# Performance work log

Hardware: AMD Instinct MI355X
Metric: run time of the kernel (lower is better)

## Reference

```python
import jax, jax.numpy as jnp
import numpy as np

N1 = 1_000_000
N2 = 1_000_000
C = 64
M = 1_500_000


def setup_inputs() -> dict:
    key = jax.random.key(0)
    k1, k2, k3, k4, k5, k6 = jax.random.split(key, 6)
    feat1 = jax.random.normal(k1, (N1, C), dtype=jnp.float32)
    feat2 = jax.random.normal(k2, (N2, C), dtype=jnp.float32)
    # union_map[0] gathers each input row exactly once -> permutation
    map1_in = jax.random.permutation(k3, N1).astype(jnp.int32)
    map2_in = jax.random.permutation(k4, N2).astype(jnp.int32)
    # union_map[1]: output row each input point lands in
    map1_out = jax.random.randint(k5, (N1,), 0, M, dtype=jnp.int32)
    map2_out = jax.random.randint(k6, (N2,), 0, M, dtype=jnp.int32)
    return {
        "feat1": feat1, "feat2": feat2,
        "map1_in": map1_in, "map1_out": map1_out,
        "map2_in": map2_in, "map2_out": map2_out,
        "out_size": M,
    }


def reference(feat1, feat2, map1_in, map1_out, map2_in, map2_out, out_size):
    # out_feat[union_map[1]] += in_feat[union_map[0]] for each input tensor
    out = jnp.zeros((out_size, feat1.shape[1]), dtype=feat1.dtype)
    out = out.at[map1_out].add(feat1[map1_in])
    out = out.at[map2_out].add(feat2[map2_in])
    return out
```

## Files before the change

kernel.cpp:

```cpp
#include <hip/hip_runtime.h>


#define ROW_C 64
#define TBIT (1 << 30)
#define CONT 0x80000000u
#define NIL  0xFFFFFFFFu
#define SCAN_T 256
#define SCAN_PER 16
#define SCAN_CHUNK (SCAN_T * SCAN_PER)

typedef float f32x4 __attribute__((ext_vector_type(4)));
typedef int   i32x4 __attribute__((ext_vector_type(4)));
typedef unsigned long long u64;

__device__ __forceinline__ f32x4 feat_load(const float* __restrict__ feat1,
                                           const float* __restrict__ feat2,
                                           int v, int sub) {
    const float* f = (v & TBIT) ? feat2 : feat1;
    int ir = v & (TBIT - 1);
    return *reinterpret_cast<const f32x4*>(f + (size_t)ir * ROW_C + sub);
}

__global__ __launch_bounds__(256) void k_fill_list(
        const int* __restrict__ m1i, const int* __restrict__ m1o,
        const int* __restrict__ m2i, const int* __restrict__ m2o,
        int n1, int n2,
        unsigned* __restrict__ head, u64* __restrict__ entries) {
    int i = blockIdx.x * blockDim.x + threadIdx.x;
    int r, v;
    if (i < n1) { r = m1o[i]; v = m1i[i]; }
    else {
        int j = i - n1;
        if (j >= n2) return;
        r = m2o[j]; v = m2i[j] | TBIT;
    }
    unsigned old = atomicExch(&head[r], (unsigned)i);
    entries[i] = ((u64)old << 32) | (unsigned)v;
}

__global__ __launch_bounds__(256) void k_compact(
        const unsigned* __restrict__ head, const u64* __restrict__ entries,
        int* __restrict__ rec, int M) {
    int r = blockIdx.x * blockDim.x + threadIdx.x;
    if (r >= M) return;
    unsigned idx = head[r];
    int s0 = -1, s1 = -1, s2 = -1, s3 = -1;
    if (idx != NIL) {
        u64 e = entries[idx];
        s0 = (int)(unsigned)e; idx = (unsigned)(e >> 32);
        if (idx != NIL) {
            e = entries[idx];
            s1 = (int)(unsigned)e; idx = (unsigned)(e >> 32);
            if (idx != NIL) {
                e = entries[idx];
                s2 = (int)(unsigned)e; idx = (unsigned)(e >> 32);
                if (idx != NIL) {
                    unsigned nx = idx;
                    e = entries[idx];
                    unsigned link = (unsigned)(e >> 32);
                    if (link == NIL) {
                        s3 = (int)(unsigned)e;
                    } else {
                        s3 = (int)(CONT | nx);
                    }
                }
            }
        }
    }
    i32x4 q = { s0, s1, s2, s3 };
    *reinterpret_cast<i32x4*>(rec + ((size_t)r << 2)) = q;
}

__global__ __launch_bounds__(256) void k_gather_rec4(
        const float* __restrict__ feat1, const float* __restrict__ feat2,
        const int* __restrict__ rec, const u64* __restrict__ entries,
        float* __restrict__ out, int M) {
    int gid = blockIdx.x * blockDim.x + threadIdx.x;
    int row = gid >> 4;
    if (row >= M) return;
    int sub = (gid & 15) << 2;

    const i32x4 s = __builtin_nontemporal_load(
        reinterpret_cast<const i32x4*>(rec + ((size_t)row << 2)));

    f32x4 acc = {0.f, 0.f, 0.f, 0.f};
    if (s.x != -1) acc += feat_load(feat1, feat2, s.x, sub);
    if (s.y != -1) acc += feat_load(feat1, feat2, s.y, sub);
    if (s.z != -1) acc += feat_load(feat1, feat2, s.z, sub);
    if (s.w != -1) {
        if ((unsigned)s.w & CONT) {
            unsigned idx = (unsigned)s.w & 0x7FFFFFFFu;
            while (idx != NIL) {
                u64 e = entries[idx];
                acc += feat_load(feat1, feat2, (int)(unsigned)e, sub);
                idx = (unsigned)(e >> 32);
            }
        } else {
            acc += feat_load(feat1, feat2, s.w, sub);
        }
    }

    __builtin_nontemporal_store(acc,
        reinterpret_cast<f32x4*>(out + (size_t)row * ROW_C + sub));
}

__global__ void k_hist(const int* __restrict__ map_out, int n, int* __restrict__ counts) {
    int i = blockIdx.x * blockDim.x + threadIdx.x;
    if (i < n) atomicAdd(&counts[map_out[i]], 1);
}

__global__ void k_partial(const int* __restrict__ counts, int M, int* __restrict__ bsum) {
    __shared__ int lds[SCAN_T];
    int base = blockIdx.x * SCAN_CHUNK + threadIdx.x * SCAN_PER;
    int s = 0;
#pragma unroll
    for (int k = 0; k < SCAN_PER; k++) { int i = base + k; if (i < M) s += counts[i]; }
    lds[threadIdx.x] = s; __syncthreads();
    for (int off = SCAN_T / 2; off > 0; off >>= 1) {
        if (threadIdx.x < off) lds[threadIdx.x] += lds[threadIdx.x + off];
        __syncthreads();
    }
    if (threadIdx.x == 0) bsum[blockIdx.x] = lds[0];
}

__global__ void k_scan_bsum(int* __restrict__ bsum, int nblk) {
    __shared__ int lds[512];
    int t = threadIdx.x;
    lds[t] = (t < nblk) ? bsum[t] : 0;
    __syncthreads();
    for (int off = 1; off < 512; off <<= 1) {
        int v = (t >= off) ? lds[t - off] : 0;
        __syncthreads();
        lds[t] += v;
        __syncthreads();
    }
    if (t < nblk) bsum[t] = (t == 0) ? 0 : lds[t - 1];
}

__global__ void k_offsets(const int* __restrict__ counts, int M,
                          const int* __restrict__ bsum, int* __restrict__ cursor) {
    __shared__ int lds[SCAN_T];
    int base = blockIdx.x * SCAN_CHUNK + threadIdx.x * SCAN_PER;
    int c[SCAN_PER]; int s = 0;
#pragma unroll
    for (int k = 0; k < SCAN_PER; k++) { int i = base + k; c[k] = (i < M) ? counts[i] : 0; s += c[k]; }
    lds[threadIdx.x] = s; __syncthreads();
    for (int off = 1; off < SCAN_T; off <<= 1) {
        int v = (threadIdx.x >= off) ? lds[threadIdx.x - off] : 0;
        __syncthreads();
        lds[threadIdx.x] += v;
        __syncthreads();
    }
    int prefix = bsum[blockIdx.x] + ((threadIdx.x == 0) ? 0 : lds[threadIdx.x - 1]);
#pragma unroll
    for (int k = 0; k < SCAN_PER; k++) { int i = base + k; if (i < M) cursor[i] = prefix; prefix += c[k]; }
}

__global__ void k_fill(const int* __restrict__ map_in, const int* __restrict__ map_out,
                       int n, int tbit, int* __restrict__ cursor, int* __restrict__ csr) {
    int i = blockIdx.x * blockDim.x + threadIdx.x;
    if (i >= n) return;
    int r = map_out[i];
    int pos = atomicAdd(&cursor[r], 1);
    csr[pos] = map_in[i] | tbit;
}

__global__ void k_gather(const float* __restrict__ feat1, const float* __restrict__ feat2,
                         const int* __restrict__ counts, const int* __restrict__ cursor,
                         const int* __restrict__ csr, float* __restrict__ out, int M) {
    int gid = blockIdx.x * blockDim.x + threadIdx.x;
    int row = gid >> 4;
    if (row >= M) return;
    int sub = (gid & 15) << 2;

    int cnt = counts[row];
    int end = cursor[row];
    int start = end - cnt;

    float4 acc = {0.f, 0.f, 0.f, 0.f};
    for (int k = 0; k < cnt; k++) {
        int e = csr[start + k];
        const float* f = (e & TBIT) ? feat2 : feat1;
        int in_r = e & (TBIT - 1);
        float4 v = *reinterpret_cast<const float4*>(f + (size_t)in_r * ROW_C + sub);
        acc.x += v.x; acc.y += v.y; acc.z += v.z; acc.w += v.w;
    }
    *reinterpret_cast<float4*>(out + (size_t)row * ROW_C + sub) = acc;
}

__global__ void scatter_add_rows(const float* __restrict__ feat,
                                 const int* __restrict__ map_in,
                                 const int* __restrict__ map_out,
                                 float* __restrict__ out,
                                 int n_rows) {
    int gid = blockIdx.x * blockDim.x + threadIdx.x;
    int row = gid >> 4;
    if (row >= n_rows) return;
    int sub = (gid & 15) << 2;
    int in_r  = map_in[row];
    int out_r = map_out[row];
    const float4 v = *reinterpret_cast<const float4*>(feat + (size_t)in_r * ROW_C + sub);
    float* o = out + (size_t)out_r * ROW_C + sub;
    unsafeAtomicAdd(o + 0, v.x);
    unsafeAtomicAdd(o + 1, v.y);
    unsafeAtomicAdd(o + 2, v.z);
    unsafeAtomicAdd(o + 3, v.w);
}

extern "C" void kernel_launch(void* const* d_in, const int* in_sizes, int n_in,
                              void* d_out, int out_size, void* d_ws, size_t ws_size,
                              hipStream_t stream) {
    const float* feat1    = (const float*)d_in[0];
    const float* feat2    = (const float*)d_in[1];
    const int*   map1_in  = (const int*)d_in[2];
    const int*   map1_out = (const int*)d_in[3];
    const int*   map2_in  = (const int*)d_in[4];
    const int*   map2_out = (const int*)d_in[5];
    float* out = (float*)d_out;

    const int n1 = in_sizes[2];
    const int n2 = in_sizes[4];
    const int M  = out_size / ROW_C;
    const int ntot = n1 + n2;
    const int block = 256;

    const size_t head_bytes = (((size_t)M * 4 + 7) & ~(size_t)7);
    const size_t need_list = head_bytes + (size_t)ntot * sizeof(u64)
                           + (size_t)M * 4 * sizeof(int);
    if (ws_size >= need_list) {
        unsigned* head = (unsigned*)d_ws;
        u64* entries   = (u64*)((char*)d_ws + head_bytes);
        int* rec       = (int*)(entries + ntot);

        (void)hipMemsetAsync(head, 0xFF, (size_t)M * sizeof(unsigned), stream);

        int gridf = (ntot + block - 1) / block;
        k_fill_list<<<gridf, block, 0, stream>>>(map1_in, map1_out, map2_in, map2_out,
                                                 n1, n2, head, entries);

        int gridc = (M + block - 1) / block;
        k_compact<<<gridc, block, 0, stream>>>(head, entries, rec, M);

        int gridg = (int)(((long long)M * 16 + block - 1) / block);
        k_gather_rec4<<<gridg, block, 0, stream>>>(feat1, feat2, rec, entries, out, M);
        return;
    }

    const int nblk = (M + SCAN_CHUNK - 1) / SCAN_CHUNK;
    const size_t need_csr = (size_t)(2 * (size_t)M + (size_t)ntot + (size_t)nblk) * sizeof(int);
    if (ws_size >= need_csr && nblk <= 512) {
        int* counts = (int*)d_ws;
        int* cursor = counts + M;
        int* csr    = cursor + M;
        int* bsum   = csr + ntot;

        (void)hipMemsetAsync(counts, 0, (size_t)M * sizeof(int), stream);
        k_hist<<<(n1 + block - 1) / block, block, 0, stream>>>(map1_out, n1, counts);
        k_hist<<<(n2 + block - 1) / block, block, 0, stream>>>(map2_out, n2, counts);
        k_partial<<<nblk, SCAN_T, 0, stream>>>(counts, M, bsum);
        k_scan_bsum<<<1, 512, 0, stream>>>(bsum, nblk);
        k_offsets<<<nblk, SCAN_T, 0, stream>>>(counts, M, bsum, cursor);
        k_fill<<<(n1 + block - 1) / block, block, 0, stream>>>(map1_in, map1_out, n1, 0, cursor, csr);
        k_fill<<<(n2 + block - 1) / block, block, 0, stream>>>(map2_in, map2_out, n2, TBIT, cursor, csr);
        int gridg = (int)(((long long)M * 16 + block - 1) / block);
        k_gather<<<gridg, block, 0, stream>>>(feat1, feat2, counts, cursor, csr, out, M);
        return;
    }

    (void)hipMemsetAsync(out, 0, (size_t)out_size * sizeof(float), stream);
    int grid1 = (int)(((long long)n1 * 16 + block - 1) / block);
    int grid2 = (int)(((long long)n2 * 16 + block - 1) / block);
    scatter_add_rows<<<grid1, block, 0, stream>>>(feat1, map1_in, map1_out, out, n1);
    scatter_add_rows<<<grid2, block, 0, stream>>>(feat2, map2_in, map2_out, out, n2);
}
```

Baseline: 330.2 us.

## Offload rows with more than four contributors to an atomic overflow pass

The compact kernel now stores the first four contributors of each output row and appends any further (row, source) pairs to an overflow list through a global atomic counter. The gather kernel no longer walks linked-list chains, which removes divergent dependent loads from the hot path. A new grid-stride kernel then adds the overflow contributions with float atomics. This costs an extra launch, a memset, and contention on one counter. Overflow beyond the fixed capacity would be silently dropped. The rec load also changes from nontemporal to a normal load.

```diff
diff --git a/kernel.cpp b/kernel.cpp
--- a/kernel.cpp
+++ b/kernel.cpp
@@ -3,8 +3,8 @@
 
 #define ROW_C 64
 #define TBIT (1 << 30)
-#define CONT 0x80000000u
 #define NIL  0xFFFFFFFFu
+#define OVF_CAP (1 << 20)
 #define SCAN_T 256
 #define SCAN_PER 16
 #define SCAN_CHUNK (SCAN_T * SCAN_PER)
@@ -40,7 +40,8 @@
 
 __global__ __launch_bounds__(256) void k_compact(
         const unsigned* __restrict__ head, const u64* __restrict__ entries,
-        int* __restrict__ rec, int M) {
+        int* __restrict__ rec, int M,
+        int* __restrict__ ovf, int* __restrict__ ovf_n) {
     int r = blockIdx.x * blockDim.x + threadIdx.x;
     if (r >= M) return;
     unsigned idx = head[r];
@@ -55,13 +56,16 @@
                 e = entries[idx];
                 s2 = (int)(unsigned)e; idx = (unsigned)(e >> 32);
                 if (idx != NIL) {
-                    unsigned nx = idx;
                     e = entries[idx];
-                    unsigned link = (unsigned)(e >> 32);
-                    if (link == NIL) {
-                        s3 = (int)(unsigned)e;
-                    } else {
-                        s3 = (int)(CONT | nx);
+                    s3 = (int)(unsigned)e; idx = (unsigned)(e >> 32);
+                    while (idx != NIL) {
+                        e = entries[idx];
+                        int p = atomicAdd(ovf_n, 1);
+                        if (p < OVF_CAP) {
+                            ovf[2 * p]     = r;
+                            ovf[2 * p + 1] = (int)(unsigned)e;
+                        }
+                        idx = (unsigned)(e >> 32);
                     }
                 }
             }
@@ -73,35 +77,42 @@
 
 __global__ __launch_bounds__(256) void k_gather_rec4(
         const float* __restrict__ feat1, const float* __restrict__ feat2,
-        const int* __restrict__ rec, const u64* __restrict__ entries,
-        float* __restrict__ out, int M) {
+        const int* __restrict__ rec, float* __restrict__ out, int M) {
     int gid = blockIdx.x * blockDim.x + threadIdx.x;
     int row = gid >> 4;
     if (row >= M) return;
     int sub = (gid & 15) << 2;
 
-    const i32x4 s = __builtin_nontemporal_load(
-        reinterpret_cast<const i32x4*>(rec + ((size_t)row << 2)));
+    const i32x4 s = *reinterpret_cast<const i32x4*>(rec + ((size_t)row << 2));
 
     f32x4 acc = {0.f, 0.f, 0.f, 0.f};
     if (s.x != -1) acc += feat_load(feat1, feat2, s.x, sub);
     if (s.y != -1) acc += feat_load(feat1, feat2, s.y, sub);
     if (s.z != -1) acc += feat_load(feat1, feat2, s.z, sub);
-    if (s.w != -1) {
-        if ((unsigned)s.w & CONT) {
-            unsigned idx = (unsigned)s.w & 0x7FFFFFFFu;
-            while (idx != NIL) {
-                u64 e = entries[idx];
-                acc += feat_load(feat1, feat2, (int)(unsigned)e, sub);
-                idx = (unsigned)(e >> 32);
-            }
-        } else {
-            acc += feat_load(feat1, feat2, s.w, sub);
-        }
-    }
+    if (s.w != -1) acc += feat_load(feat1, feat2, s.w, sub);
 
     __builtin_nontemporal_store(acc,
         reinterpret_cast<f32x4*>(out + (size_t)row * ROW_C + sub));
+}
+
+__global__ void k_overflow(const int* __restrict__ ovf_n, const int* __restrict__ ovf,
+                           const float* __restrict__ feat1, const float* __restrict__ feat2,
+                           float* __restrict__ out) {
+    int total = *ovf_n;
+    if (total > OVF_CAP) total = OVF_CAP;
+    int stride = gridDim.x * blockDim.x;
+    for (int idx = blockIdx.x * blockDim.x + threadIdx.x; idx < total * 16; idx += stride) {
+        int e = idx >> 4;
+        int sub = (idx & 15) << 2;
+        int r = ovf[2 * e];
+        int v = ovf[2 * e + 1];
+        f32x4 x = feat_load(feat1, feat2, v, sub);
+        float* o = out + (size_t)r * ROW_C + sub;
+        unsafeAtomicAdd(o + 0, x.x);
+        unsafeAtomicAdd(o + 1, x.y);
+        unsafeAtomicAdd(o + 2, x.z);
+        unsafeAtomicAdd(o + 3, x.w);
+    }
 }
 
 __global__ void k_hist(const int* __restrict__ map_out, int n, int* __restrict__ counts) {
@@ -225,13 +236,17 @@
     const int block = 256;
 
     const size_t head_bytes = (((size_t)M * 4 + 7) & ~(size_t)7);
-    const size_t need_list = head_bytes + (size_t)ntot * sizeof(u64)
-                           + (size_t)M * 4 * sizeof(int);
+    const size_t need_list = 64 + head_bytes + (size_t)ntot * sizeof(u64)
+                           + (size_t)M * 4 * sizeof(int)
+                           + 2 * (size_t)OVF_CAP * sizeof(int);
     if (ws_size >= need_list) {
-        unsigned* head = (unsigned*)d_ws;
-        u64* entries   = (u64*)((char*)d_ws + head_bytes);
-        int* rec       = (int*)(entries + ntot);
-
+        int*      hdr     = (int*)d_ws;
+        unsigned* head    = (unsigned*)((char*)d_ws + 64);
+        u64*      entries = (u64*)((char*)d_ws + 64 + head_bytes);
+        int*      rec     = (int*)(entries + ntot);
+        int*      ovf     = rec + (size_t)M * 4;
+
+        (void)hipMemsetAsync(hdr, 0, 64, stream);
         (void)hipMemsetAsync(head, 0xFF, (size_t)M * sizeof(unsigned), stream);
 
         int gridf = (ntot + block - 1) / block;
@@ -239,10 +254,12 @@
                                                  n1, n2, head, entries);
 
         int gridc = (M + block - 1) / block;
-        k_compact<<<gridc, block, 0, stream>>>(head, entries, rec, M);
+        k_compact<<<gridc, block, 0, stream>>>(head, entries, rec, M, ovf, hdr);
 
         int gridg = (int)(((long long)M * 16 + block - 1) / block);
-        k_gather_rec4<<<gridg, block, 0, stream>>>(feat1, feat2, rec, entries, out, M);
+        k_gather_rec4<<<gridg, block, 0, stream>>>(feat1, feat2, rec, out, M);
+
+        k_overflow<<<512, block, 0, stream>>>(hdr, ovf, feat1, feat2, out);
         return;
     }
 
```

After: 521.9 us. +58.0%, slower.
